# Optimization experiments

Hardware: AMD Instinct MI355X
Metric: run time of the kernel (lower is better)

## Reference

```python
import jax, jax.numpy as jnp
import numpy as np


def setup_inputs() -> dict:
    key = jax.random.key(0)
    k1, k2, k3 = jax.random.split(key, 3)
    B, U, D0, D1 = 256, 512, 512, 1024
    x = jax.random.normal(k1, (B, D0), dtype=jnp.float32)
    y = jax.random.normal(k2, (B, D1), dtype=jnp.float32)
    # Glorot-uniform-ish scale for the bilinear weight
    limit = np.sqrt(6.0 / (D0 + D1)).astype(np.float32)
    w = jax.random.uniform(k3, (U, D0, D1), dtype=jnp.float32, minval=-limit, maxval=limit)
    b = jnp.zeros((U,), dtype=jnp.float32)
    return {"x": x, "y": y, "w": w, "b": b}


def reference(x, y, w, b):
    # out[b,u] = sum_{i,j} x[b,i] * w[u,i,j] * y[b,j] + b[u]
    # Two chained GEMMs instead of materializing (B,U,D0,D1):
    xw = jnp.einsum('bi,uij->buj', x, w)   # (B, U, D1)
    out = jnp.einsum('buj,bj->bu', xw, y) + b  # (B, U)
    return out
```

## Files before the change

### kernel.cpp

```cpp
#include <hip/hip_runtime.h>
#include <hip/hip_bf16.h>

typedef float f32x4 __attribute__((ext_vector_type(4)));
typedef short s16x8 __attribute__((ext_vector_type(8)));

#define NB   256
#define NU   512
#define ND0  512
#define ND1  1024
#define WROW (ND0 * ND1)

__device__ __forceinline__ unsigned int f2bf_pk(float a, float b) {
  __hip_bfloat16 ha = __float2bfloat16(a);
  __hip_bfloat16 hb = __float2bfloat16(b);
  unsigned short ua, ub;
  __builtin_memcpy(&ua, &ha, 2);
  __builtin_memcpy(&ub, &hb, 2);
  return (unsigned int)ua | ((unsigned int)ub << 16);
}

__device__ __forceinline__ void block_sync_lds() {
  asm volatile("s_waitcnt lgkmcnt(0)" ::: "memory");
  __builtin_amdgcn_s_barrier();
}

__global__ __launch_bounds__(256) void init_out(const float* __restrict__ bias,
                                                float* __restrict__ out) {
  int idx = blockIdx.x * 256 + threadIdx.x;
  out[idx] = bias[idx & (NU - 1)];
}

__global__ __launch_bounds__(512, 4) void bilinear_kern(
    const float* __restrict__ x, const float* __restrict__ y,
    const float* __restrict__ w, float* __restrict__ out) {
  __shared__ char Alds[32768];
  __shared__ char Wlds[16384];

  const int t    = threadIdx.x;
  const int lane = t & 63;
  const int l15  = lane & 15;
  const int lk   = lane >> 4;
  const int wid  = t >> 6;
  const int wm   = wid >> 2;
  const int wn   = wid & 3;

  const int nt    = blockIdx.x & 3;
  const int ic    = blockIdx.x >> 2;
  const int ucol0 = nt * 128 + wn * 32;

  f32x4 acc[8][2];
#pragma unroll
  for (int mf = 0; mf < 8; ++mf)
#pragma unroll
    for (int nf = 0; nf < 2; ++nf)
#pragma unroll
      for (int r = 0; r < 4; ++r) acc[mf][nf][r] = 0.0f;

  const int ar   = t >> 4;
  const int aswz = (ar & 7) << 4;
  const int awr  = ar * 128 + ((l15 * 8) ^ aswz);
  const float* yb = y + (size_t)ar * ND1 + l15 * 4;

  const int wrb = wid * 16 + lk;
  const float* wq = w + (size_t)(nt * 128 + wrb) * WROW + l15 * 4;

  const int afswz = (l15 & 7) << 4;

  f32x4 wv[4], wvn[4];
  {
    const float* p0 = wq + (size_t)(ic * 4) * ND1;
#pragma unroll
    for (int q = 0; q < 4; ++q)
      wv[q] = *(const f32x4*)(p0 + (size_t)q * 4 * WROW);
  }
  float xv[8];
#pragma unroll
  for (int p = 0; p < 8; ++p)
    xv[p] = x[(size_t)(ar + 32 * p) * ND0 + ic * 4];

  for (int it = 0; it < 64; ++it) {
    const int j0 = (it & 15) * 64;

    block_sync_lds();

#pragma unroll
    for (int g = 0; g < 2; ++g) {
      f32x4 v[4];
#pragma unroll
      for (int pp = 0; pp < 4; ++pp)
        v[pp] = *(const f32x4*)(yb + (size_t)(g * 4 + pp) * 32 * ND1 + j0);
#pragma unroll
      for (int pp = 0; pp < 4; ++pp) {
        const int p = g * 4 + pp;
        unsigned long long pk =
            (unsigned long long)f2bf_pk(xv[p] * v[pp][0], xv[p] * v[pp][1]) |
            ((unsigned long long)f2bf_pk(xv[p] * v[pp][2], xv[p] * v[pp][3]) << 32);
        *(unsigned long long*)(Alds + awr + p * 4096) = pk;
      }
    }

#pragma unroll
    for (int q = 0; q < 4; ++q) {
      const int row  = wrb + 4 * q;
      const int byte = row * 128 + ((l15 * 8) ^ ((row & 7) << 4));
      unsigned long long pk =
          (unsigned long long)f2bf_pk(wv[q][0], wv[q][1]) |
          ((unsigned long long)f2bf_pk(wv[q][2], wv[q][3]) << 32);
      *(unsigned long long*)(Wlds + byte) = pk;
    }

    if (it < 63) {
      const int tn = it + 1;
      const int ii = ic * 4 + (tn >> 4);
      const int jn = (tn & 15) * 64;
      const float* pn = wq + (size_t)ii * ND1 + jn;
#pragma unroll
      for (int q = 0; q < 4; ++q)
        wvn[q] = *(const f32x4*)(pn + (size_t)q * 4 * WROW);
      if ((it & 15) == 15) {
#pragma unroll
        for (int pp = 0; pp < 8; ++pp)
          xv[pp] = x[(size_t)(ar + 32 * pp) * ND0 + ii];
      }
    }

    block_sync_lds();

#pragma unroll
    for (int ks = 0; ks < 2; ++ks) {
      const int kcol = ks * 64;
      s16x8 bf[2];
#pragma unroll
      for (int nf = 0; nf < 2; ++nf) {
        const int row = wn * 32 + nf * 16 + l15;
        bf[nf] = *(const s16x8*)(Wlds + row * 128 + ((kcol + lk * 16) ^ afswz));
      }
#pragma unroll
      for (int mf = 0; mf < 8; ++mf) {
        const int row = wm * 128 + mf * 16 + l15;
        s16x8 af = *(const s16x8*)(Alds + row * 128 + ((kcol + lk * 16) ^ afswz));
        acc[mf][0] = __builtin_amdgcn_mfma_f32_16x16x32_bf16(af, bf[0], acc[mf][0], 0, 0, 0);
        acc[mf][1] = __builtin_amdgcn_mfma_f32_16x16x32_bf16(af, bf[1], acc[mf][1], 0, 0, 0);
      }
    }

#pragma unroll
    for (int q = 0; q < 4; ++q) wv[q] = wvn[q];
  }

#pragma unroll
  for (int mf = 0; mf < 8; ++mf) {
    const int grow = wm * 128 + mf * 16 + lk * 4;
#pragma unroll
    for (int nf = 0; nf < 2; ++nf) {
      const int gcol = ucol0 + nf * 16 + l15;
#pragma unroll
      for (int r = 0; r < 4; ++r) {
        atomicAdd(out + (size_t)(grow + r) * NU + gcol, acc[mf][nf][r]);
      }
    }
  }
}

extern "C" void kernel_launch(void* const* d_in, const int* in_sizes, int n_in,
                              void* d_out, int out_size, void* d_ws, size_t ws_size,
                              hipStream_t stream) {
  const float* x    = (const float*)d_in[0];
  const float* y    = (const float*)d_in[1];
  const float* w    = (const float*)d_in[2];
  const float* bias = (const float*)d_in[3];
  float* out = (float*)d_out;

  init_out<<<512, 256, 0, stream>>>(bias, out);
  bilinear_kern<<<512, 512, 0, stream>>>(x, y, w, out);
}
```

Measured before the change: 310.6 us.

## Stagger per-block iteration start and ping-pong W prefetch registers

Each block now begins its 64-step K loop at a rotated offset derived from its tile and chunk index, so that concurrent blocks read different y columns and W rows at any given moment. The loop is unrolled by two with alternating wvA/wvB register buffers, which removes the end-of-iteration register copy. The order of issue is also changed: all eight y loads go out before the W LDS stores and the next-W prefetch, to hide more global latency. The rotation is meant to reduce hot spots in the memory channels, cache contention and clustered atomic adds, at the cost of higher register pressure from holding eight y vectors at once.

```diff
diff --git a/kernel.cpp b/kernel.cpp
--- a/kernel.cpp
+++ b/kernel.cpp
@@ -46,6 +46,7 @@
 
   const int nt    = blockIdx.x & 3;
   const int ic    = blockIdx.x >> 2;
+  const int off   = (nt << 4) | (ic & 15);
   const int ucol0 = nt * 128 + wn * 32;
 
   f32x4 acc[8][2];
@@ -66,87 +67,96 @@
 
   const int afswz = (l15 & 7) << 4;
 
-  f32x4 wv[4], wvn[4];
+  f32x4 wvA[4], wvB[4];
+  float xv[8];
   {
-    const float* p0 = wq + (size_t)(ic * 4) * ND1;
+    const int s0  = off;
+    const int ii0 = ic * 4 + (s0 >> 4);
+    const int j00 = (s0 & 15) * 64;
+    const float* p0 = wq + (size_t)ii0 * ND1 + j00;
 #pragma unroll
     for (int q = 0; q < 4; ++q)
-      wv[q] = *(const f32x4*)(p0 + (size_t)q * 4 * WROW);
+      wvA[q] = *(const f32x4*)(p0 + (size_t)q * 4 * WROW);
+#pragma unroll
+    for (int p = 0; p < 8; ++p)
+      xv[p] = x[(size_t)(ar + 32 * p) * ND0 + ii0];
   }
-  float xv[8];
-#pragma unroll
-  for (int p = 0; p < 8; ++p)
-    xv[p] = x[(size_t)(ar + 32 * p) * ND0 + ic * 4];
 
-  for (int it = 0; it < 64; ++it) {
-    const int j0 = (it & 15) * 64;
+#define BODY(IT, WCUR, WNXT)                                                  \
+  {                                                                           \
+    const int s  = ((IT) + off) & 63;                                         \
+    const int j0 = (s & 15) * 64;                                             \
+    block_sync_lds();            \
+                     \
+    f32x4 v[8];                                                               \
+    _Pragma("unroll")                                                         \
+    for (int p = 0; p < 8; ++p)                                               \
+      v[p] = *(const f32x4*)(yb + (size_t)p * 32 * ND1 + j0);                 \
+        \
+        \
+    _Pragma("unroll")                                                         \
+    for (int q = 0; q < 4; ++q) {                                             \
+      const int row  = wrb + 4 * q;                                           \
+      const int byte = row * 128 + ((l15 * 8) ^ ((row & 7) << 4));            \
+      unsigned long long pk =                                                 \
+          (unsigned long long)f2bf_pk(WCUR[q][0], WCUR[q][1]) |               \
+          ((unsigned long long)f2bf_pk(WCUR[q][2], WCUR[q][3]) << 32);        \
+      *(unsigned long long*)(Wlds + byte) = pk;                               \
+    }                                                                         \
+         \
+         \
+    if ((IT) < 63) {                                                          \
+      const int sn  = (s + 1) & 63;                                           \
+      const int iin = ic * 4 + (sn >> 4);                                     \
+      const int jn  = (sn & 15) * 64;                                         \
+      const float* pn = wq + (size_t)iin * ND1 + jn;                          \
+      _Pragma("unroll")                                                       \
+      for (int q = 0; q < 4; ++q)                                             \
+        WNXT[q] = *(const f32x4*)(pn + (size_t)q * 4 * WROW);                 \
+    }                                                                         \
+                   \
+    _Pragma("unroll")                                                         \
+    for (int p = 0; p < 8; ++p) {                                             \
+      unsigned long long pk =                                                 \
+          (unsigned long long)f2bf_pk(xv[p] * v[p][0], xv[p] * v[p][1]) |     \
+          ((unsigned long long)f2bf_pk(xv[p] * v[p][2], xv[p] * v[p][3])      \
+           << 32);                                                            \
+      *(unsigned long long*)(Alds + awr + p * 4096) = pk;                     \
+    }                                                                         \
+        \
+       \
+    if ((IT) < 63 && (s & 15) == 15) {                                        \
+      const int iin = ic * 4 + (((s + 1) & 63) >> 4);                         \
+      _Pragma("unroll")                                                       \
+      for (int pp = 0; pp < 8; ++pp)                                          \
+        xv[pp] = x[(size_t)(ar + 32 * pp) * ND0 + iin];                       \
+    }                                                                         \
+    block_sync_lds();             \
+                                 \
+    _Pragma("unroll")                                                         \
+    for (int ks = 0; ks < 2; ++ks) {                                          \
+      const int kcol = ks * 64;                                               \
+      s16x8 bfr[2];                                                           \
+      _Pragma("unroll")                                                       \
+      for (int nf = 0; nf < 2; ++nf) {                                        \
+        const int row = wn * 32 + nf * 16 + l15;                              \
+        bfr[nf] = *(const s16x8*)(Wlds + row * 128 + ((kcol + lk * 16) ^ afswz)); \
+      }                                                                       \
+      _Pragma("unroll")                                                       \
+      for (int mf = 0; mf < 8; ++mf) {                                        \
+        const int row = wm * 128 + mf * 16 + l15;                             \
+        s16x8 af = *(const s16x8*)(Alds + row * 128 + ((kcol + lk * 16) ^ afswz)); \
+        acc[mf][0] = __builtin_amdgcn_mfma_f32_16x16x32_bf16(af, bfr[0], acc[mf][0], 0, 0, 0); \
+        acc[mf][1] = __builtin_amdgcn_mfma_f32_16x16x32_bf16(af, bfr[1], acc[mf][1], 0, 0, 0); \
+      }                                                                       \
+    }                                                                         \
+  }
 
-    block_sync_lds();
-
-#pragma unroll
-    for (int g = 0; g < 2; ++g) {
-      f32x4 v[4];
-#pragma unroll
-      for (int pp = 0; pp < 4; ++pp)
-        v[pp] = *(const f32x4*)(yb + (size_t)(g * 4 + pp) * 32 * ND1 + j0);
-#pragma unroll
-      for (int pp = 0; pp < 4; ++pp) {
-        const int p = g * 4 + pp;
-        unsigned long long pk =
-            (unsigned long long)f2bf_pk(xv[p] * v[pp][0], xv[p] * v[pp][1]) |
-            ((unsigned long long)f2bf_pk(xv[p] * v[pp][2], xv[p] * v[pp][3]) << 32);
-        *(unsigned long long*)(Alds + awr + p * 4096) = pk;
-      }
-    }
-
-#pragma unroll
-    for (int q = 0; q < 4; ++q) {
-      const int row  = wrb + 4 * q;
-      const int byte = row * 128 + ((l15 * 8) ^ ((row & 7) << 4));
-      unsigned long long pk =
-          (unsigned long long)f2bf_pk(wv[q][0], wv[q][1]) |
-          ((unsigned long long)f2bf_pk(wv[q][2], wv[q][3]) << 32);
-      *(unsigned long long*)(Wlds + byte) = pk;
-    }
-
-    if (it < 63) {
-      const int tn = it + 1;
-      const int ii = ic * 4 + (tn >> 4);
-      const int jn = (tn & 15) * 64;
-      const float* pn = wq + (size_t)ii * ND1 + jn;
-#pragma unroll
-      for (int q = 0; q < 4; ++q)
-        wvn[q] = *(const f32x4*)(pn + (size_t)q * 4 * WROW);
-      if ((it & 15) == 15) {
-#pragma unroll
-        for (int pp = 0; pp < 8; ++pp)
-          xv[pp] = x[(size_t)(ar + 32 * pp) * ND0 + ii];
-      }
-    }
-
-    block_sync_lds();
-
-#pragma unroll
-    for (int ks = 0; ks < 2; ++ks) {
-      const int kcol = ks * 64;
-      s16x8 bf[2];
-#pragma unroll
-      for (int nf = 0; nf < 2; ++nf) {
-        const int row = wn * 32 + nf * 16 + l15;
-        bf[nf] = *(const s16x8*)(Wlds + row * 128 + ((kcol + lk * 16) ^ afswz));
-      }
-#pragma unroll
-      for (int mf = 0; mf < 8; ++mf) {
-        const int row = wm * 128 + mf * 16 + l15;
-        s16x8 af = *(const s16x8*)(Alds + row * 128 + ((kcol + lk * 16) ^ afswz));
-        acc[mf][0] = __builtin_amdgcn_mfma_f32_16x16x32_bf16(af, bf[0], acc[mf][0], 0, 0, 0);
-        acc[mf][1] = __builtin_amdgcn_mfma_f32_16x16x32_bf16(af, bf[1], acc[mf][1], 0, 0, 0);
-      }
-    }
-
-#pragma unroll
-    for (int q = 0; q < 4; ++q) wv[q] = wvn[q];
+  for (int ot = 0; ot < 32; ++ot) {
+    BODY(2 * ot,     wvA, wvB)
+    BODY(2 * ot + 1, wvB, wvA)
   }
+#undef BODY
 
 #pragma unroll
   for (int mf = 0; mf < 8; ++mf) {
```

After: 544.2 us. 75.2% more time.
